# Performance work log

Measured on AMD Instinct MI355X. Metric: run time of the kernel, lower is better.

## Reference

```python
import jax, jax.numpy as jnp
import numpy as np

N_GROUPS = 32
EPS = 1e-6


def group_norm(x, gamma, beta):
    # x: (b, c, h, w); 32 groups, eps=1e-6, affine
    b, c, h, w = x.shape
    xg = x.reshape(b, N_GROUPS, c // N_GROUPS, h, w)
    mean = xg.mean(axis=(2, 3, 4), keepdims=True)
    var = xg.var(axis=(2, 3, 4), keepdims=True)
    xg = (xg - mean) * jax.lax.rsqrt(var + EPS)
    x = xg.reshape(b, c, h, w)
    return x * gamma[None, :, None, None] + beta[None, :, None, None]


def setup_inputs() -> dict:
    key = jax.random.key(0)
    ks = jax.random.split(key, 8)
    b, c, h, w = 4, 512, 64, 64
    sc = 1.0 / np.sqrt(c)
    return {
        "x": jax.random.normal(ks[0], (b, c, h, w), jnp.float32),
        "gn_w": jnp.ones((c,), jnp.float32),
        "gn_b": jnp.zeros((c,), jnp.float32),
        "wq": jax.random.normal(ks[1], (c, c), jnp.float32) * sc,
        "bq": jnp.zeros((c,), jnp.float32),
        "wk": jax.random.normal(ks[2], (c, c), jnp.float32) * sc,
        "bk": jnp.zeros((c,), jnp.float32),
        "wv": jax.random.normal(ks[3], (c, c), jnp.float32) * sc,
        "bv": jnp.zeros((c,), jnp.float32),
        "wo": jax.random.normal(ks[4], (c, c), jnp.float32) * sc,
        "bo": jnp.zeros((c,), jnp.float32),
    }


def reference(x, gn_w, gn_b, wq, bq, wk, bk, wv, bv, wo, bo):
    b, c, h, w = x.shape
    s = c ** (-0.5)
    xn = group_norm(x, gn_w, gn_b)
    xf = xn.reshape(b, c, h * w)  # (b, c, hw)
    # 1x1 convs == channel matmuls: weight (out_c, in_c)
    q = jnp.einsum('oc,bci->boi', wq, xf) + bq[None, :, None]
    k = jnp.einsum('oc,bci->boi', wk, xf) + bk[None, :, None]
    v = jnp.einsum('oc,bci->boi', wv, xf) + bv[None, :, None]
    attn = jnp.einsum('bci,bcj->bij', q, k) * s  # (b, hw, hw)
    attn = jax.nn.softmax(attn, axis=-1)
    out = jnp.einsum('bij,bcj->bci', attn, v)  # (b, c, hw)
    out = jnp.einsum('oc,bci->boi', wo, out) + bo[None, :, None]
    return out.reshape(b, c, h, w) + x
```

## Files before the change

kernel.cpp:

```cpp
#include <hip/hip_runtime.h>

#define B 4
#define C 512
#define HW 4096
#define NG 32
#define GSZ 65536
#define KROW 528

typedef unsigned short u16;
typedef unsigned int u32;
typedef __attribute__((ext_vector_type(8))) short short8;
typedef __attribute__((ext_vector_type(4))) float f32x4;

__device__ __forceinline__ float bf2f(u16 u) {
    union { u32 i; float f; } x; x.i = ((u32)u) << 16; return x.f;
}
__device__ __forceinline__ u16 f2bf(float f) {
    union { u32 i; float f; } x; x.f = f;
    u32 r = x.i + 0x7FFF + ((x.i >> 16) & 1);
    return (u16)(r >> 16);
}
__device__ __forceinline__ u32 cvtpk(float lo, float hi) {
    u32 r;
    asm("v_cvt_pk_bf16_f32 %0, %1, %2" : "=v"(r) : "v"(lo), "v"(hi));
    return r;
}

__device__ __forceinline__ void gld16(const u16* g, u16* l) {
    __builtin_amdgcn_global_load_lds(
        (const __attribute__((address_space(1))) void*)g,
        (__attribute__((address_space(3))) void*)l, 16, 0, 0);
}

__global__ __launch_bounds__(256) void conv_kernel(
        const float* __restrict__ wq, const float* __restrict__ wk,
        const float* __restrict__ wv, const float* __restrict__ wo,
        u16* __restrict__ dst) {
    const int mat = blockIdx.y;
    const float* src = (mat == 0) ? wq : (mat == 1) ? wk : (mat == 2) ? wv : wo;
    const int idx = (blockIdx.x * 256 + threadIdx.x) * 4;
    float4 v = *(const float4*)(src + idx);
    uint2 r = make_uint2(cvtpk(v.x, v.y), cvtpk(v.z, v.w));
    *(uint2*)(dst + (size_t)mat * (C * C) + idx) = r;
}

__global__ __launch_bounds__(256) void gn_stats_kernel(
        const float* __restrict__ x, float2* __restrict__ part) {
    const int gl = blockIdx.x;
    const int qt = blockIdx.y;
    const size_t base = (size_t)gl * GSZ + (size_t)qt * (GSZ / 4);
    const int tid = threadIdx.x;
    float s = 0.f, s2 = 0.f;
    for (int i = tid * 4; i < GSZ / 4; i += 1024) {
        float4 v4 = *(const float4*)(x + base + i);
        s  += v4.x + v4.y + v4.z + v4.w;
        s2 += v4.x*v4.x + v4.y*v4.y + v4.z*v4.z + v4.w*v4.w;
    }
    #pragma unroll
    for (int off = 32; off > 0; off >>= 1) {
        s  += __shfl_down(s, off, 64);
        s2 += __shfl_down(s2, off, 64);
    }
    __shared__ float rs[4], rs2[4];
    int lane = tid & 63, wid = tid >> 6;
    if (lane == 0) { rs[wid] = s; rs2[wid] = s2; }
    __syncthreads();
    if (tid == 0) {
        part[gl * 4 + qt] = make_float2(rs[0] + rs[1] + rs[2] + rs[3],
                                        rs2[0] + rs2[1] + rs2[2] + rs2[3]);
    }
}

__global__ __launch_bounds__(256) void gn_apply_kernel(
        const float* __restrict__ x, const float* __restrict__ gamma,
        const float* __restrict__ beta, const float2* __restrict__ part,
        u16* __restrict__ xnT) {
    const int b = blockIdx.y;
    const int i0 = blockIdx.x * 32;
    const int tid = threadIdx.x;
    __shared__ float gm[512], bt[512];
    __shared__ __align__(16) u16 tile[32 * 512];

    for (int c = tid; c < 512; c += 256) {
        int g = c >> 4;
        const float2* pp = part + ((size_t)b * 32 + g) * 4;
        float2 p0 = pp[0], p1 = pp[1], p2 = pp[2], p3 = pp[3];
        float mean = (p0.x + p1.x + p2.x + p3.x) * (1.f / GSZ);
        float var  = (p0.y + p1.y + p2.y + p3.y) * (1.f / GSZ) - mean * mean;
        float rstd = rsqrtf(var + 1e-6f);
        float gg = gamma[c] * rstd;
        gm[c] = gg;
        bt[c] = beta[c] - mean * gg;
    }
    __syncthreads();
    const int ci = tid >> 5;
    const int ii = tid & 31;
    const float* xb = x + (size_t)b * 512 * 4096 + i0;
    #pragma unroll 4
    for (int p = 0; p < 64; p++) {
        int c = p * 8 + ci;
        float v = xb[(size_t)c * 4096 + ii] * gm[c] + bt[c];
        tile[ii * 512 + (c ^ ((ii & 7) << 3))] = f2bf(v);
    }
    __syncthreads();
    u16* dst = xnT + ((size_t)b * HW + i0) * C;
    #pragma unroll
    for (int p = 0; p < 8; p++) {
        int i = p * 4 + (tid >> 6);
        int ch = tid & 63;
        *(uint4*)(dst + (size_t)i * C + ch * 8) =
            *(const uint4*)&tile[i * 512 + ((ch ^ (i & 7)) << 3)];
    }
}

__global__ __launch_bounds__(256) void qkv_kernel(
        const u16* __restrict__ xnT, const u16* __restrict__ wb,
        const float* __restrict__ bq, const float* __restrict__ bk,
        const float* __restrict__ bv,
        u16* __restrict__ qT, u16* __restrict__ kT, u16* __restrict__ vimg) {
    const int mat = blockIdx.y >> 2;
    const int oT0 = (blockIdx.y & 3) * 128;
    const int iT0 = blockIdx.x * 128;
    const int b = blockIdx.z;
    const u16* Ag = xnT + ((size_t)b * HW + iT0) * C;
    const u16* Bg = wb + (size_t)mat * C * C + (size_t)oT0 * C;
    const float* bias = (mat == 0) ? bq : (mat == 1) ? bk : bv;

    const int tid = threadIdx.x;
    const int w = tid >> 6, lane = tid & 63;
    const int qd = lane >> 4, nn = lane & 15;
    const int wm = w & 1, wn = w >> 1;

    __shared__ __align__(16) u16 smem[16384];
    u16* As0 = smem;
    u16* Bs0 = smem + 8192;

    f32x4 acc[4][4];
    #pragma unroll
    for (int mt = 0; mt < 4; mt++)
        #pragma unroll
        for (int nt = 0; nt < 4; nt++) acc[mt][nt] = (f32x4){0.f, 0.f, 0.f, 0.f};

    auto stage = [&](u16* dst, const u16* g, int c0) {
        #pragma unroll
        for (int p = 0; p < 2; p++) {
            int rbase = 32 * w + 16 * p;
            int row = rbase + (lane >> 2);
            gld16(g + (size_t)row * C + c0 + (((lane & 3) ^ ((row >> 1) & 3)) << 3),
                  dst + rbase * 32);
        }
    };

    stage(As0, Ag, 0);
    stage(Bs0, Bg, 0);

    for (int kt = 0; kt < 16; kt++) {
        const int cur = kt & 1;
        __syncthreads();
        if (kt < 15) {
            stage(As0 + (cur ^ 1) * 4096, Ag, (kt + 1) * 32);
            stage(Bs0 + (cur ^ 1) * 4096, Bg, (kt + 1) * 32);
        }
        const u16* Ac = As0 + cur * 4096;
        const u16* Bc = Bs0 + cur * 4096;
        short8 af[4], bf[4];
        #pragma unroll
        for (int mt = 0; mt < 4; mt++) {
            int row = 64 * wm + 16 * mt + nn;
            af[mt] = *(const short8*)&Ac[row * 32 + ((qd ^ ((row >> 1) & 3)) << 3)];
        }
        #pragma unroll
        for (int nt = 0; nt < 4; nt++) {
            int row = 64 * wn + 16 * nt + nn;
            bf[nt] = *(const short8*)&Bc[row * 32 + ((qd ^ ((row >> 1) & 3)) << 3)];
        }
        #pragma unroll
        for (int mt = 0; mt < 4; mt++)
            #pragma unroll
            for (int nt = 0; nt < 4; nt++)
                acc[mt][nt] = __builtin_amdgcn_mfma_f32_16x16x32_bf16(af[mt], bf[nt], acc[mt][nt], 0, 0, 0);
    }

    __syncthreads();
    u16* dt = smem;

    if (mat < 2) {
        #pragma unroll
        for (int nt = 0; nt < 4; nt++) {
            int o_l = 64 * wn + 16 * nt + nn;
            float bb = bias[oT0 + o_l];
            #pragma unroll
            for (int mt = 0; mt < 4; mt++) {
                int i_l = 64 * wm + 16 * mt + qd * 4;
                dt[(i_l + 0) * 128 + o_l] = f2bf(acc[mt][nt][0] + bb);
                dt[(i_l + 1) * 128 + o_l] = f2bf(acc[mt][nt][1] + bb);
                dt[(i_l + 2) * 128 + o_l] = f2bf(acc[mt][nt][2] + bb);
                dt[(i_l + 3) * 128 + o_l] = f2bf(acc[mt][nt][3] + bb);
            }
        }
        __syncthreads();
        u16* dstT = ((mat == 0) ? qT : kT) + ((size_t)b * HW + iT0) * C + oT0;
        #pragma unroll
        for (int p = 0; p < 8; p++) {
            int i_l = p * 16 + (tid >> 4);
            int ch = tid & 15;
            *(uint4*)(dstT + (size_t)i_l * C + ch * 8) = *(const uint4*)&dt[i_l * 128 + ch * 8];
        }
    } else {
        #pragma unroll
        for (int nt = 0; nt < 4; nt++) {
            int c_l = 64 * wn + 16 * nt + nn;
            float bb = bias[oT0 + c_l];
            #pragma unroll
            for (int mt = 0; mt < 4; mt++) {
                int i_l = 64 * wm + 16 * mt + qd * 4;
                int lc = i_l >> 5;
                int j0 = i_l & 31;
                union { uint2 u; ushort4 s; } st;
                st.u = make_uint2(cvtpk(acc[mt][nt][0] + bb, acc[mt][nt][1] + bb),
                                  cvtpk(acc[mt][nt][2] + bb, acc[mt][nt][3] + bb));
                *(ushort4*)&dt[lc * 4096 + c_l * 32 +
                               (((j0 >> 3) ^ ((c_l >> 2) & 3)) << 3) + (j0 & 7)] = st.s;
            }
        }
        __syncthreads();
        u16* vb = vimg + (size_t)b * 128 * 16384;
        const int chb = iT0 >> 5;
        #pragma unroll
        for (int p = 0; p < 8; p++) {
            int lc = p >> 1, half = p & 1;
            *(uint4*)(vb + (size_t)(chb + lc) * 16384 + oT0 * 32 + half * 2048 + tid * 8) =
                *(const uint4*)&dt[lc * 4096 + half * 2048 + tid * 8];
        }
    }
}

__global__ __launch_bounds__(512, 2) void attn_kernel(
        const u16* __restrict__ qT, const u16* __restrict__ kT,
        const u16* __restrict__ vimg, u16* __restrict__ oT) {
    const int b = blockIdx.y;
    const int i0 = blockIdx.x * 64;
    const int tid = threadIdx.x;
    const int w = tid >> 6;
    const int lane = tid & 63;
    const int q = lane >> 4;
    const int n = lane & 15;
    const int rw = w & 3;
    const int jh = w >> 2;

    __shared__ __align__(16) u16 kbuf[2][32 * KROW];
    __shared__ __align__(16) u16 pbuf[2][64 * 40];
    __shared__ __align__(16) float mflag[2][8];
    __shared__ __align__(16) float lpart[2][64];

    short8 qf[16];
    {
        const u16* qrow = qT + ((size_t)b * HW + i0 + rw * 16 + n) * C + q * 8;
        #pragma unroll
        for (int k = 0; k < 16; k++) {
            uint4 u = *(const uint4*)(qrow + k * 32);
            qf[k] = *(const short8*)&u;
        }
    }
    f32x4 oacc[4][4];
    #pragma unroll
    for (int mt = 0; mt < 4; mt++)
        #pragma unroll
        for (int ct = 0; ct < 4; ct++)
            oacc[mt][ct] = (f32x4){0.f, 0.f, 0.f, 0.f};
    float mreg = 0.f;
    float lsum[4] = {0.f, 0.f, 0.f, 0.f};

    const u16* kTb = kT + (size_t)b * HW * C;
    const u16* vTb = vimg + (size_t)b * 128 * 16384;

    auto stageK = [&](int gc, int buf) {
        const u16* gk = kTb + (size_t)gc * 32 * C;
        #pragma unroll
        for (int ii = 0; ii < 4; ii++) {
            int j = w * 4 + ii;
            gld16(gk + (size_t)j * C + ((lane ^ (j & 7)) << 3), &kbuf[buf][j * KROW]);
        }
    };

    const float scale = 0.04419417382415922f;
    stageK(0, 0);
    stageK(1, 1);
    __syncthreads();

    auto s_phase = [&](int slot, int par, float alpha) {
        f32x4 s0 = {0.f,0.f,0.f,0.f}, s1 = {0.f,0.f,0.f,0.f};
        f32x4 s2 = {0.f,0.f,0.f,0.f}, s3 = {0.f,0.f,0.f,0.f};
        const int sw = n & 7;
        const u16* kb = kbuf[slot] + (jh * 16 + n) * KROW;
        __builtin_amdgcn_s_setprio(1);
        #pragma unroll
        for (int m = 0; m < 4; m++) {
            short8 b0 = *(const short8*)&kb[(((4 * m + 0) * 4 + q) ^ sw) << 3];
            short8 b1 = *(const short8*)&kb[(((4 * m + 1) * 4 + q) ^ sw) << 3];
            short8 b2 = *(const short8*)&kb[(((4 * m + 2) * 4 + q) ^ sw) << 3];
            short8 b3 = *(const short8*)&kb[(((4 * m + 3) * 4 + q) ^ sw) << 3];
            s0 = __builtin_amdgcn_mfma_f32_16x16x32_bf16(qf[4 * m + 0], b0, s0, 0, 0, 0);
            s1 = __builtin_amdgcn_mfma_f32_16x16x32_bf16(qf[4 * m + 1], b1, s1, 0, 0, 0);
            s2 = __builtin_amdgcn_mfma_f32_16x16x32_bf16(qf[4 * m + 2], b2, s2, 0, 0, 0);
            s3 = __builtin_amdgcn_mfma_f32_16x16x32_bf16(qf[4 * m + 3], b3, s3, 0, 0, 0);
        }
        __builtin_amdgcn_s_setprio(0);
        float sv[4];
        #pragma unroll
        for (int r = 0; r < 4; r++) sv[r] = ((s0[r] + s1[r]) + (s2[r] + s3[r])) * scale;
        float pm = fmaxf(fmaxf(sv[0], sv[1]), fmaxf(sv[2], sv[3]));
        float flagv = -1e30f;
        if (__any(pm > mreg + 8.0f)) {
            float mx = pm;
            mx = fmaxf(mx, __shfl_xor(mx, 1));
            mx = fmaxf(mx, __shfl_xor(mx, 2));
            mx = fmaxf(mx, __shfl_xor(mx, 4));
            mx = fmaxf(mx, __shfl_xor(mx, 8));
            mx = fmaxf(mx, __shfl_xor(mx, 16));
            mx = fmaxf(mx, __shfl_xor(mx, 32));
            flagv = mx;
        }
        if (lane == 0) mflag[par][w] = flagv;
        float p0 = __expf(sv[0] - mreg), p1 = __expf(sv[1] - mreg);
        float p2 = __expf(sv[2] - mreg), p3 = __expf(sv[3] - mreg);
        lsum[0] = lsum[0] * alpha + p0;
        lsum[1] = lsum[1] * alpha + p1;
        lsum[2] = lsum[2] * alpha + p2;
        lsum[3] = lsum[3] * alpha + p3;
        u32 a = cvtpk(p0, p1), c = cvtpk(p2, p3);
        u16* pb = &pbuf[par][(rw * 16 + q * 4) * 40 + jh * 16 + n];
        pb[0]      = (u16)a;
        pb[40]     = (u16)(a >> 16);
        pb[80]     = (u16)c;
        pb[120]    = (u16)(c >> 16);
    };

    s_phase(0, 0, 1.f);
    __syncthreads();

    #pragma unroll 1
    for (int t = 0; t < 128; ++t) {
        const int cur = t & 1;
        f32x4 fl0 = *(const f32x4*)&mflag[cur][0];
        f32x4 fl1 = *(const f32x4*)&mflag[cur][4];
        short8 pf[4];
        #pragma unroll
        for (int mt = 0; mt < 4; mt++)
            pf[mt] = *(const short8*)&pbuf[cur][(mt * 16 + n) * 40 + q * 8];
        uint4 vpf[4];
        {
            const u16* gv = vTb + (size_t)t * 16384;
            #pragma unroll
            for (int ct = 0; ct < 4; ct++) {
                int c = w * 64 + ct * 16 + n;
                vpf[ct] = *(const uint4*)&gv[c * 32 + ((q ^ ((c >> 2) & 3)) << 3)];
            }
        }
        if (t < 126) stageK(t + 2, cur);
        float mnew = mreg;
        #pragma unroll
        for (int i = 0; i < 4; i++) mnew = fmaxf(mnew, fmaxf(fl0[i], fl1[i]));
        float alpha = 1.f;
        if (mnew > mreg) { alpha = __expf(mreg - mnew); mreg = mnew; }
        if (t < 127) {
            s_phase(cur ^ 1, cur ^ 1, alpha);
        } else {
            #pragma unroll
            for (int r = 0; r < 4; r++) lsum[r] *= alpha;
        }
        __builtin_amdgcn_s_setprio(1);
        #pragma unroll
        for (int ct = 0; ct < 4; ct++) {
            short8 vf = *(const short8*)&vpf[ct];
            #pragma unroll
            for (int mt = 0; mt < 4; mt++)
                oacc[mt][ct] = __builtin_amdgcn_mfma_f32_16x16x32_bf16(pf[mt], vf, oacc[mt][ct], 0, 0, 0);
        }
        __builtin_amdgcn_s_setprio(0);
        if (alpha != 1.f) {
            #pragma unroll
            for (int mt = 0; mt < 4; mt++)
                #pragma unroll
                for (int ct = 0; ct < 4; ct++) {
                    oacc[mt][ct][0] *= alpha; oacc[mt][ct][1] *= alpha;
                    oacc[mt][ct][2] *= alpha; oacc[mt][ct][3] *= alpha;
                }
        }
        __syncthreads();
    }
    #pragma unroll
    for (int r = 0; r < 4; r++) {
        float l = lsum[r];
        l += __shfl_xor(l, 1);
        l += __shfl_xor(l, 2);
        l += __shfl_xor(l, 4);
        l += __shfl_xor(l, 8);
        if (n == 0) lpart[jh][rw * 16 + q * 4 + r] = l;
    }
    __syncthreads();
    #pragma unroll
    for (int mt = 0; mt < 4; mt++) {
        float inv[4];
        #pragma unroll
        for (int r = 0; r < 4; r++) {
            int row = mt * 16 + q * 4 + r;
            inv[r] = 1.f / (lpart[0][row] + lpart[1][row]);
        }
        #pragma unroll
        for (int ct = 0; ct < 4; ct++) {
            int cc = w * 64 + ct * 16 + n;
            size_t base = ((size_t)b * HW + i0 + mt * 16 + q * 4) * C + cc;
            oT[base        ] = f2bf(oacc[mt][ct][0] * inv[0]);
            oT[base +   C  ] = f2bf(oacc[mt][ct][1] * inv[1]);
            oT[base + 2 * C] = f2bf(oacc[mt][ct][2] * inv[2]);
            oT[base + 3 * C] = f2bf(oacc[mt][ct][3] * inv[3]);
        }
    }
}

__global__ __launch_bounds__(256) void proj_kernel(
        const u16* __restrict__ oT, const u16* __restrict__ wob,
        const float* __restrict__ bo, const float* __restrict__ x,
        float* __restrict__ out) {
    const int o0 = blockIdx.y * 128;
    const int i0t = blockIdx.x * 128;
    const int b = blockIdx.z;
    const u16* Ag = wob + (size_t)o0 * C;
    const u16* Bg = oT + ((size_t)b * HW + i0t) * C;

    const int tid = threadIdx.x;
    const int w = tid >> 6, lane = tid & 63;
    const int qd = lane >> 4, nn = lane & 15;
    const int wm = w & 1, wn = w >> 1;

    __shared__ __align__(16) u16 As[2][128 * 32];
    __shared__ __align__(16) u16 Bs[2][128 * 32];

    f32x4 acc[4][4];
    #pragma unroll
    for (int mt = 0; mt < 4; mt++)
        #pragma unroll
        for (int nt = 0; nt < 4; nt++) acc[mt][nt] = (f32x4){0.f, 0.f, 0.f, 0.f};

    auto stage = [&](u16* dst, const u16* g, int c0) {
        #pragma unroll
        for (int p = 0; p < 2; p++) {
            int rbase = 32 * w + 16 * p;
            int row = rbase + (lane >> 2);
            gld16(g + (size_t)row * C + c0 + (((lane & 3) ^ ((row >> 1) & 3)) << 3),
                  dst + rbase * 32);
        }
    };

    stage(As[0], Ag, 0);
    stage(Bs[0], Bg, 0);

    for (int kt = 0; kt < 16; kt++) {
        const int cur = kt & 1;
        __syncthreads();
        if (kt < 15) {
            stage(As[cur ^ 1], Ag, (kt + 1) * 32);
            stage(Bs[cur ^ 1], Bg, (kt + 1) * 32);
        }
        short8 af[4], bf[4];
        #pragma unroll
        for (int mt = 0; mt < 4; mt++) {
            int row = 64 * wm + 16 * mt + nn;
            af[mt] = *(const short8*)&As[cur][row * 32 + ((qd ^ ((row >> 1) & 3)) << 3)];
        }
        #pragma unroll
        for (int nt = 0; nt < 4; nt++) {
            int row = 64 * wn + 16 * nt + nn;
            bf[nt] = *(const short8*)&Bs[cur][row * 32 + ((qd ^ ((row >> 1) & 3)) << 3)];
        }
        #pragma unroll
        for (int mt = 0; mt < 4; mt++)
            #pragma unroll
            for (int nt = 0; nt < 4; nt++)
                acc[mt][nt] = __builtin_amdgcn_mfma_f32_16x16x32_bf16(af[mt], bf[nt], acc[mt][nt], 0, 0, 0);
    }

    #pragma unroll
    for (int mt = 0; mt < 4; mt++) {
        #pragma unroll
        for (int r = 0; r < 4; r++) {
            int o = o0 + 64 * wm + 16 * mt + qd * 4 + r;
            float bb = bo[o];
            #pragma unroll
            for (int nt = 0; nt < 4; nt++) {
                int i = i0t + 64 * wn + 16 * nt + nn;
                size_t idx = ((size_t)b * C + o) * HW + i;
                out[idx] = acc[mt][nt][r] + bb + x[idx];
            }
        }
    }
}

extern "C" void kernel_launch(void* const* d_in, const int* in_sizes, int n_in,
                              void* d_out, int out_size, void* d_ws, size_t ws_size,
                              hipStream_t stream) {
    const float* x    = (const float*)d_in[0];
    const float* gn_w = (const float*)d_in[1];
    const float* gn_b = (const float*)d_in[2];
    const float* wq   = (const float*)d_in[3];
    const float* bq   = (const float*)d_in[4];
    const float* wk   = (const float*)d_in[5];
    const float* bk   = (const float*)d_in[6];
    const float* wv   = (const float*)d_in[7];
    const float* bv   = (const float*)d_in[8];
    const float* wo   = (const float*)d_in[9];
    const float* bo   = (const float*)d_in[10];
    float* out = (float*)d_out;

    const size_t WSZ = (size_t)C * C;
    const size_t S1  = (size_t)B * C * HW;
    u16* wb    = (u16*)d_ws;
    u16* wob   = wb + 3 * WSZ;
    u16* xnT   = wob + WSZ;
    u16* qT    = xnT + S1;
    u16* kT    = qT + S1;
    u16* vimg  = kT + S1;
    u16* oT    = vimg + S1;
    float2* part = (float2*)(oT + S1);

    hipLaunchKernelGGL(conv_kernel,     dim3(256, 4), dim3(256), 0, stream, wq, wk, wv, wo, wb);
    hipLaunchKernelGGL(gn_stats_kernel, dim3(B*NG, 4), dim3(256), 0, stream, x, part);
    hipLaunchKernelGGL(gn_apply_kernel, dim3(HW/32, B), dim3(256), 0, stream,
                       x, gn_w, gn_b, part, xnT);
    hipLaunchKernelGGL(qkv_kernel,      dim3(HW/128, 12, B), dim3(256), 0, stream,
                       xnT, wb, bq, bk, bv, qT, kT, vimg);
    hipLaunchKernelGGL(attn_kernel,     dim3(HW/64, B), dim3(512), 0, stream,
                       qT, kT, vimg, oT);
    hipLaunchKernelGGL(proj_kernel,     dim3(HW/128, C/128, B), dim3(256), 0, stream, oT, wob, bo, x, out);
}
```

Measured before the change: 366.0 us.

## Process two key chunks per attention iteration and merge weight-convert with GN stats

The attention loop now handles two 32-key chunks per iteration over a 4-deep K ring buffer. This halves the number of block barriers and max-flag exchanges, and the running-max update is shared across the pair. The K rows drop their padding (KROW 528 to 512), so the kernel relies on the XOR swizzle alone to avoid bank conflicts. Separately, the weight bf16 conversion and group-norm statistics kernels are fused into one launch to save a kernel launch. The cost is more LDS per block (4 K buffers, wider P buffer), which could reduce occupancy at 2 blocks of 512 threads.

```diff
diff --git a/kernel.cpp b/kernel.cpp
--- a/kernel.cpp
+++ b/kernel.cpp
@@ -5,7 +5,6 @@
 #define HW 4096
 #define NG 32
 #define GSZ 65536
-#define KROW 528
 
 typedef unsigned short u16;
 typedef unsigned int u32;
@@ -32,24 +31,26 @@
         (__attribute__((address_space(3))) void*)l, 16, 0, 0);
 }
 
-__global__ __launch_bounds__(256) void conv_kernel(
+__global__ __launch_bounds__(256) void prep_kernel(
         const float* __restrict__ wq, const float* __restrict__ wk,
         const float* __restrict__ wv, const float* __restrict__ wo,
-        u16* __restrict__ dst) {
-    const int mat = blockIdx.y;
-    const float* src = (mat == 0) ? wq : (mat == 1) ? wk : (mat == 2) ? wv : wo;
-    const int idx = (blockIdx.x * 256 + threadIdx.x) * 4;
-    float4 v = *(const float4*)(src + idx);
-    uint2 r = make_uint2(cvtpk(v.x, v.y), cvtpk(v.z, v.w));
-    *(uint2*)(dst + (size_t)mat * (C * C) + idx) = r;
-}
-
-__global__ __launch_bounds__(256) void gn_stats_kernel(
-        const float* __restrict__ x, float2* __restrict__ part) {
-    const int gl = blockIdx.x;
-    const int qt = blockIdx.y;
+        u16* __restrict__ dst, const float* __restrict__ x,
+        float2* __restrict__ part) {
+    const int bid = blockIdx.x;
+    const int tid = threadIdx.x;
+    if (bid < 1024) {
+        const int mat = bid >> 8;
+        const float* src = (mat == 0) ? wq : (mat == 1) ? wk : (mat == 2) ? wv : wo;
+        const int idx = ((bid & 255) * 256 + tid) * 4;
+        float4 v = *(const float4*)(src + idx);
+        uint2 r = make_uint2(cvtpk(v.x, v.y), cvtpk(v.z, v.w));
+        *(uint2*)(dst + (size_t)mat * (C * C) + idx) = r;
+        return;
+    }
+    const int idx2 = bid - 1024;
+    const int gl = idx2 >> 2;
+    const int qt = idx2 & 3;
     const size_t base = (size_t)gl * GSZ + (size_t)qt * (GSZ / 4);
-    const int tid = threadIdx.x;
     float s = 0.f, s2 = 0.f;
     for (int i = tid * 4; i < GSZ / 4; i += 1024) {
         float4 v4 = *(const float4*)(x + base + i);
@@ -248,8 +249,8 @@
     const int rw = w & 3;
     const int jh = w >> 2;
 
-    __shared__ __align__(16) u16 kbuf[2][32 * KROW];
-    __shared__ __align__(16) u16 pbuf[2][64 * 40];
+    __shared__ __align__(16) u16 kbuf[4][32 * 512];
+    __shared__ __align__(16) u16 pbuf[2][64 * 72];
     __shared__ __align__(16) float mflag[2][8];
     __shared__ __align__(16) float lpart[2][64];
 
@@ -274,25 +275,23 @@
     const u16* kTb = kT + (size_t)b * HW * C;
     const u16* vTb = vimg + (size_t)b * 128 * 16384;
 
-    auto stageK = [&](int gc, int buf) {
+    auto stageK = [&](int gc) {
         const u16* gk = kTb + (size_t)gc * 32 * C;
+        u16* kb = kbuf[gc & 3];
         #pragma unroll
         for (int ii = 0; ii < 4; ii++) {
             int j = w * 4 + ii;
-            gld16(gk + (size_t)j * C + ((lane ^ (j & 7)) << 3), &kbuf[buf][j * KROW]);
+            gld16(gk + (size_t)j * C + ((lane ^ (j & 7)) << 3), &kb[j * 512]);
         }
     };
 
     const float scale = 0.04419417382415922f;
-    stageK(0, 0);
-    stageK(1, 1);
-    __syncthreads();
-
-    auto s_phase = [&](int slot, int par, float alpha) {
+
+    auto s_phase = [&](int c, int par, float alpha) -> float {
         f32x4 s0 = {0.f,0.f,0.f,0.f}, s1 = {0.f,0.f,0.f,0.f};
         f32x4 s2 = {0.f,0.f,0.f,0.f}, s3 = {0.f,0.f,0.f,0.f};
         const int sw = n & 7;
-        const u16* kb = kbuf[slot] + (jh * 16 + n) * KROW;
+        const u16* kb = kbuf[c & 3] + (jh * 16 + n) * 512;
         __builtin_amdgcn_s_setprio(1);
         #pragma unroll
         for (int m = 0; m < 4; m++) {
@@ -310,6 +309,22 @@
         #pragma unroll
         for (int r = 0; r < 4; r++) sv[r] = ((s0[r] + s1[r]) + (s2[r] + s3[r])) * scale;
         float pm = fmaxf(fmaxf(sv[0], sv[1]), fmaxf(sv[2], sv[3]));
+        float p0 = __expf(sv[0] - mreg), p1 = __expf(sv[1] - mreg);
+        float p2 = __expf(sv[2] - mreg), p3 = __expf(sv[3] - mreg);
+        lsum[0] = lsum[0] * alpha + p0;
+        lsum[1] = lsum[1] * alpha + p1;
+        lsum[2] = lsum[2] * alpha + p2;
+        lsum[3] = lsum[3] * alpha + p3;
+        u32 a = cvtpk(p0, p1), cc = cvtpk(p2, p3);
+        u16* pb = &pbuf[par][(rw * 16 + q * 4) * 72 + (c & 1) * 32 + jh * 16 + n];
+        pb[0]      = (u16)a;
+        pb[72]     = (u16)(a >> 16);
+        pb[144]    = (u16)cc;
+        pb[216]    = (u16)(cc >> 16);
+        return pm;
+    };
+
+    auto wave_max = [&](float pm) -> float {
         float flagv = -1e30f;
         if (__any(pm > mreg + 8.0f)) {
             float mx = pm;
@@ -321,61 +336,80 @@
             mx = fmaxf(mx, __shfl_xor(mx, 32));
             flagv = mx;
         }
-        if (lane == 0) mflag[par][w] = flagv;
-        float p0 = __expf(sv[0] - mreg), p1 = __expf(sv[1] - mreg);
-        float p2 = __expf(sv[2] - mreg), p3 = __expf(sv[3] - mreg);
-        lsum[0] = lsum[0] * alpha + p0;
-        lsum[1] = lsum[1] * alpha + p1;
-        lsum[2] = lsum[2] * alpha + p2;
-        lsum[3] = lsum[3] * alpha + p3;
-        u32 a = cvtpk(p0, p1), c = cvtpk(p2, p3);
-        u16* pb = &pbuf[par][(rw * 16 + q * 4) * 40 + jh * 16 + n];
-        pb[0]      = (u16)a;
-        pb[40]     = (u16)(a >> 16);
-        pb[80]     = (u16)c;
-        pb[120]    = (u16)(c >> 16);
+        return flagv;
     };
 
-    s_phase(0, 0, 1.f);
+    stageK(0); stageK(1); stageK(2); stageK(3);
+    __syncthreads();
+    {
+        float pm_a = s_phase(0, 0, 1.f);
+        float pm_b = s_phase(1, 0, 1.f);
+        float flagv = wave_max(fmaxf(pm_a, pm_b));
+        if (lane == 0) mflag[0][w] = flagv;
+    }
     __syncthreads();
 
     #pragma unroll 1
-    for (int t = 0; t < 128; ++t) {
+    for (int t = 0; t < 64; ++t) {
         const int cur = t & 1;
         f32x4 fl0 = *(const f32x4*)&mflag[cur][0];
         f32x4 fl1 = *(const f32x4*)&mflag[cur][4];
-        short8 pf[4];
+        short8 pfa[4];
         #pragma unroll
         for (int mt = 0; mt < 4; mt++)
-            pf[mt] = *(const short8*)&pbuf[cur][(mt * 16 + n) * 40 + q * 8];
-        uint4 vpf[4];
+            pfa[mt] = *(const short8*)&pbuf[cur][(mt * 16 + n) * 72 + q * 8];
+        uint4 vfa[4];
         {
-            const u16* gv = vTb + (size_t)t * 16384;
+            const u16* gv = vTb + ((size_t)2 * t) * 16384;
             #pragma unroll
             for (int ct = 0; ct < 4; ct++) {
                 int c = w * 64 + ct * 16 + n;
-                vpf[ct] = *(const uint4*)&gv[c * 32 + ((q ^ ((c >> 2) & 3)) << 3)];
+                vfa[ct] = *(const uint4*)&gv[c * 32 + ((q ^ ((c >> 2) & 3)) << 3)];
             }
         }
-        if (t < 126) stageK(t + 2, cur);
+        if (t < 62) { stageK(2 * t + 4); stageK(2 * t + 5); }
         float mnew = mreg;
         #pragma unroll
         for (int i = 0; i < 4; i++) mnew = fmaxf(mnew, fmaxf(fl0[i], fl1[i]));
         float alpha = 1.f;
         if (mnew > mreg) { alpha = __expf(mreg - mnew); mreg = mnew; }
-        if (t < 127) {
-            s_phase(cur ^ 1, cur ^ 1, alpha);
+        float flagv = -1e30f;
+        if (t < 63) {
+            float pm_a = s_phase(2 * t + 2, cur ^ 1, alpha);
+            float pm_b = s_phase(2 * t + 3, cur ^ 1, 1.f);
+            flagv = wave_max(fmaxf(pm_a, pm_b));
         } else {
             #pragma unroll
             for (int r = 0; r < 4; r++) lsum[r] *= alpha;
         }
+        if (lane == 0) mflag[cur ^ 1][w] = flagv;
+        short8 pfb[4];
+        #pragma unroll
+        for (int mt = 0; mt < 4; mt++)
+            pfb[mt] = *(const short8*)&pbuf[cur][(mt * 16 + n) * 72 + 32 + q * 8];
+        uint4 vfb[4];
+        {
+            const u16* gv = vTb + ((size_t)(2 * t + 1)) * 16384;
+            #pragma unroll
+            for (int ct = 0; ct < 4; ct++) {
+                int c = w * 64 + ct * 16 + n;
+                vfb[ct] = *(const uint4*)&gv[c * 32 + ((q ^ ((c >> 2) & 3)) << 3)];
+            }
+        }
         __builtin_amdgcn_s_setprio(1);
         #pragma unroll
         for (int ct = 0; ct < 4; ct++) {
-            short8 vf = *(const short8*)&vpf[ct];
+            short8 vf = *(const short8*)&vfa[ct];
             #pragma unroll
             for (int mt = 0; mt < 4; mt++)
-                oacc[mt][ct] = __builtin_amdgcn_mfma_f32_16x16x32_bf16(pf[mt], vf, oacc[mt][ct], 0, 0, 0);
+                oacc[mt][ct] = __builtin_amdgcn_mfma_f32_16x16x32_bf16(pfa[mt], vf, oacc[mt][ct], 0, 0, 0);
+        }
+        #pragma unroll
+        for (int ct = 0; ct < 4; ct++) {
+            short8 vf = *(const short8*)&vfb[ct];
+            #pragma unroll
+            for (int mt = 0; mt < 4; mt++)
+                oacc[mt][ct] = __builtin_amdgcn_mfma_f32_16x16x32_bf16(pfb[mt], vf, oacc[mt][ct], 0, 0, 0);
         }
         __builtin_amdgcn_s_setprio(0);
         if (alpha != 1.f) {
@@ -524,8 +558,8 @@
     u16* oT    = vimg + S1;
     float2* part = (float2*)(oT + S1);
 
-    hipLaunchKernelGGL(conv_kernel,     dim3(256, 4), dim3(256), 0, stream, wq, wk, wv, wo, wb);
-    hipLaunchKernelGGL(gn_stats_kernel, dim3(B*NG, 4), dim3(256), 0, stream, x, part);
+    hipLaunchKernelGGL(prep_kernel,     dim3(1536), dim3(256), 0, stream,
+                       wq, wk, wv, wo, wb, x, part);
     hipLaunchKernelGGL(gn_apply_kernel, dim3(HW/32, B), dim3(256), 0, stream,
                        x, gn_w, gn_b, part, xnT);
     hipLaunchKernelGGL(qkv_kernel,      dim3(HW/128, 12, B), dim3(256), 0, stream,
```

Result: no change. 366.7 us (+0.2%).
